# Optimization experiments

Hardware: AMD Instinct MI355X
Metric: run time of the kernel (lower is better)

The kernel has to match this reference:

```python
import jax, jax.numpy as jnp
import numpy as np

RADIUS = 1.0 / 16.0
MAX_NEIGHBORS = 64  # forward() passes max_num_neighbors=64
N_POINTS = 16384
N_CLOUDS = 8


def _radius_neighbors(pos, batch, r, k):
    """Dense radius graph: for each point, up to k in-radius same-cloud neighbors.
    Returns idx [N,k] int32 and mask [N,k] bool. loop=True -> self always valid."""
    sq = jnp.sum(pos * pos, axis=-1)                        # [N]
    d2 = sq[:, None] + sq[None, :] - 2.0 * (pos @ pos.T)    # [N,N]
    d2 = jnp.maximum(d2, 0.0)
    valid = (d2 <= r * r) & (batch[:, None] == batch[None, :])
    score = jnp.where(valid, -d2, -jnp.inf)
    vals, idx = jax.lax.top_k(score, k)                     # nearest-first, [N,k]
    mask = vals > -jnp.inf
    return idx, mask


def _point_conv(x, pos, idx, mask, W1, b1, W2, b2):
    """PointNetConv: msg = relu(Linear([x_j, pos_j - pos_i])), max-agg, Linear."""
    xj = x[idx]                                   # [N,K,c_in]  gather
    rel = pos[idx] - pos[:, None, :]              # [N,K,3]
    h = jnp.concatenate([xj, rel], axis=-1) @ W1 + b1   # [N,K,c_mid]
    h = jax.nn.relu(h)
    h = jnp.where(mask[..., None], h, -jnp.inf)
    agg = jnp.max(h, axis=1)                      # [N,c_mid]  max aggregation
    agg = jnp.where(jnp.isfinite(agg), agg, 0.0)  # safety (loop=True makes this moot)
    return agg @ W2 + b2                          # [N,c_out]


def setup_inputs() -> dict:
    key = jax.random.key(0)
    ks = jax.random.split(key, 16)
    pos = jax.random.uniform(ks[0], (N_POINTS, 3), dtype=jnp.float32)
    rgb = jax.random.uniform(ks[1], (N_POINTS, 3), dtype=jnp.float32)
    batch = jnp.sort(jax.random.randint(ks[2], (N_POINTS,), 0, N_CLOUDS)).astype(jnp.int64)

    def lin(k, fan_in, fan_out):
        kw, kb = jax.random.split(k)
        bound = 1.0 / np.sqrt(fan_in)
        W = jax.random.uniform(kw, (fan_in, fan_out), jnp.float32, -bound, bound)
        b = jax.random.uniform(kb, (fan_out,), jnp.float32, -bound, bound)
        return W, b

    W1a, b1a = lin(ks[3], 3 + 3, 8)
    W2a, b2a = lin(ks[4], 8, 8)
    W1b, b1b = lin(ks[5], 8 + 3, 16)
    W2b, b2b = lin(ks[6], 16, 16)
    W1c, b1c = lin(ks[7], 16 + 3, 32)
    W2c, b2c = lin(ks[8], 32, 32)
    return {"pos": pos, "rgb": rgb, "batch": batch,
            "W1a": W1a, "b1a": b1a, "W2a": W2a, "b2a": b2a,
            "W1b": W1b, "b1b": b1b, "W2b": W2b, "b2b": b2b,
            "W1c": W1c, "b1c": b1c, "W2c": W2c, "b2c": b2c}


def reference(pos, rgb, batch,
              W1a, b1a, W2a, b2a,
              W1b, b1b, W2b, b2b,
              W1c, b1c, W2c, b2c):
    # NOTE: rgb is accepted by the original forward() but never used.
    idx, mask = _radius_neighbors(pos, batch, RADIUS, MAX_NEIGHBORS)
    out = jax.nn.celu(_point_conv(pos, pos, idx, mask, W1a, b1a, W2a, b2a))
    out = jax.nn.celu(_point_conv(out, pos, idx, mask, W1b, b1b, W2b, b2b))
    out = jax.nn.celu(_point_conv(out, pos, idx, mask, W1c, b1c, W2c, b2c))
    return pos, out, batch
```

## Files before the change

kernel.cpp:

```cpp
#include <hip/hip_runtime.h>
#include <math.h>

#define N_POINTS 16384
#define CELLS_PER_CLOUD 4096
#define N_CELLS 32768
#define CAP 16
#define NBR_STRIDE 32

constexpr double R2D = 1.0 / 256.0;

__global__ __launch_bounds__(256) void k_prep(const float* __restrict__ pos,
                                              const int* __restrict__ batch,
                                              float* __restrict__ out,
                                              int* __restrict__ cnt,
                                              float4* __restrict__ bucket,
                                              float4* __restrict__ pos4)
{
    int i = blockIdx.x * 256 + threadIdx.x;
    out[i]                = pos[i];
    out[i + N_POINTS]     = pos[i + N_POINTS];
    out[i + 2 * N_POINTS] = pos[i + 2 * N_POINTS];
    out[3 * N_POINTS + 32 * N_POINTS + i] = (float)batch[i];

    float x = pos[3 * i], y = pos[3 * i + 1], z = pos[3 * i + 2];
    int ix = min(max((int)(x * 16.f), 0), 15);
    int iy = min(max((int)(y * 16.f), 0), 15);
    int iz = min(max((int)(z * 16.f), 0), 15);
    int cell = ((batch[i] * 16 + iz) * 16 + iy) * 16 + ix;
    pos4[i] = make_float4(x, y, z, __int_as_float(cell));
    int slot = atomicAdd(&cnt[cell], 1);
    if (slot < CAP) bucket[cell * CAP + slot] = make_float4(x, y, z, __int_as_float(i));
}

__global__ __launch_bounds__(64) void k_search_a(
    const float4* __restrict__ pos4,
    const int* __restrict__ cnt, const float4* __restrict__ bucket,
    const float* __restrict__ W1, const float* __restrict__ b1,
    const float* __restrict__ W2, const float* __restrict__ b2,
    float* __restrict__ out_a, float4* __restrict__ nbr, int* __restrict__ nbr_cnt)
{
    __shared__ float sW1[48], sB1[8], sW2[64], sB2[8];
    __shared__ float4 s_hits[NBR_STRIDE][64];
    int t = threadIdx.x;
    if (t < 48) sW1[t] = W1[t];
    if (t < 8) { sB1[t] = b1[t]; sB2[t] = b2[t]; }
    sW2[t] = W2[t];
    __syncthreads();

    int i = blockIdx.x * 64 + t;
    float4 pi4 = pos4[i];
    float xi = pi4.x, yi = pi4.y, zi = pi4.z;
    double xd = (double)xi, yd = (double)yi, zd = (double)zi;
    int cell0 = __float_as_int(pi4.w);
    int ix = cell0 & 15, iy = (cell0 >> 4) & 15, iz = (cell0 >> 8) & 15;
    int cb = cell0 & ~(CELLS_PER_CLOUD - 1);

    int n[27], cid[27];
#pragma unroll
    for (int c = 0; c < 27; c++) {
        int dz = c / 9 - 1, dy = (c / 3) % 3 - 1, dx = c % 3 - 1;
        int zz = iz + dz, yy = iy + dy, xx = ix + dx;
        bool ok = ((zz | yy | xx) >= 0) & (zz < 16) & (yy < 16) & (xx < 16);
        int zc = min(max(zz, 0), 15), yc = min(max(yy, 0), 15),
            xc = min(max(xx, 0), 15);
        cid[c] = cb + (zc << 8) + (yc << 4) + xc;
        int nc = min(cnt[cid[c]], CAP);
        n[c] = ok ? nc : 0;
    }
    int nmax = 0;
#pragma unroll
    for (int c = 0; c < 27; c++) nmax = max(nmax, n[c]);

    int k = 0;
    for (int s = 0; s < nmax; s++) {
#pragma unroll
        for (int c = 0; c < 27; c++) {
            if (s < n[c]) {
                float4 q = bucket[cid[c] * CAP + s];
                double ddx = xd - (double)q.x, ddy = yd - (double)q.y,
                       ddz = zd - (double)q.z;
                double d2 = ddx * ddx + ddy * ddy + ddz * ddz;
                if (d2 <= R2D) {
                    if (k < NBR_STRIDE) s_hits[k][t] = q;
                    k++;
                }
            }
        }
    }
    int kc = min(k, NBR_STRIDE);
    nbr_cnt[i] = kc;

    float mx[8];
#pragma unroll
    for (int m = 0; m < 8; m++) mx[m] = 0.f;
    for (int kk = 0; kk < kc; kk++) {
        float4 q = s_hits[kk][t];
        nbr[i * NBR_STRIDE + kk] = q;
        float in6[6] = { q.x, q.y, q.z, q.x - xi, q.y - yi, q.z - zi };
#pragma unroll
        for (int m = 0; m < 8; m++) {
            float h = sB1[m];
#pragma unroll
            for (int c6 = 0; c6 < 6; c6++) h = fmaf(in6[c6], sW1[c6 * 8 + m], h);
            mx[m] = fmaxf(mx[m], fmaxf(h, 0.f));
        }
    }

#pragma unroll
    for (int m = 0; m < 8; m++) {
        float o = sB2[m];
#pragma unroll
        for (int kk = 0; kk < 8; kk++) o = fmaf(mx[kk], sW2[kk * 8 + m], o);
        out_a[i * 8 + m] = o > 0.f ? o : expm1f(o);
    }
}

template<int CIN4, int CMID, int PTS>
__global__ __launch_bounds__(256) void k_conv(
    const float4* __restrict__ pos4, const float4* __restrict__ xin4,
    const float4* __restrict__ nbr, const int* __restrict__ nbr_cnt,
    const float* __restrict__ W1, const float* __restrict__ b1,
    const float* __restrict__ W2, const float* __restrict__ b2,
    float* __restrict__ xout)
{
    constexpr int CIN = CIN4 * 4;
    __shared__ float s_agg[PTS * CMID];
    int p = threadIdx.x / CMID;
    int m = threadIdx.x % CMID;
    int i = blockIdx.x * PTS + p;

    float4 pi = pos4[i];
    int cnt = nbr_cnt[i];

    float w1c[CIN + 3];
#pragma unroll
    for (int k = 0; k < CIN + 3; k++) w1c[k] = W1[k * CMID + m];
    float w2c[CMID];
#pragma unroll
    for (int k = 0; k < CMID; k++) w2c[k] = W2[k * CMID + m];
    float bb = b1[m];

    float mxv = 0.f;
    for (int t = 0; t < cnt; t++) {
        float4 q = nbr[i * NBR_STRIDE + t];
        int j = __float_as_int(q.w);
        float h = bb;
#pragma unroll
        for (int k = 0; k < CIN4; k++) {
            float4 v = xin4[j * CIN4 + k];
            h = fmaf(v.x, w1c[4 * k],     h);
            h = fmaf(v.y, w1c[4 * k + 1], h);
            h = fmaf(v.z, w1c[4 * k + 2], h);
            h = fmaf(v.w, w1c[4 * k + 3], h);
        }
        h = fmaf(q.x - pi.x, w1c[CIN],     h);
        h = fmaf(q.y - pi.y, w1c[CIN + 1], h);
        h = fmaf(q.z - pi.z, w1c[CIN + 2], h);
        mxv = fmaxf(mxv, fmaxf(h, 0.f));
    }
    s_agg[p * CMID + m] = mxv;
    __syncthreads();

    float o = b2[m];
#pragma unroll
    for (int k = 0; k < CMID; k++) o = fmaf(s_agg[p * CMID + k], w2c[k], o);
    xout[i * CMID + m] = o > 0.f ? o : expm1f(o);
}

extern "C" void kernel_launch(void* const* d_in, const int* in_sizes, int n_in,
                              void* d_out, int out_size, void* d_ws, size_t ws_size,
                              hipStream_t stream)
{
    const float* pos   = (const float*)d_in[0];
    const int*   batch = (const int*)d_in[2];
    const float* W1a = (const float*)d_in[3];
    const float* b1a = (const float*)d_in[4];
    const float* W2a = (const float*)d_in[5];
    const float* b2a = (const float*)d_in[6];
    const float* W1b = (const float*)d_in[7];
    const float* b1b = (const float*)d_in[8];
    const float* W2b = (const float*)d_in[9];
    const float* b2b = (const float*)d_in[10];
    const float* W1c = (const float*)d_in[11];
    const float* b1c = (const float*)d_in[12];
    const float* W2c = (const float*)d_in[13];
    const float* b2c = (const float*)d_in[14];

    float* out = (float*)d_out;

    char* ws = (char*)d_ws;
    size_t off = 0;
    auto alloc = [&](size_t bytes) {
        char* p = ws + off; off += (bytes + 255) & ~size_t(255); return p;
    };
    int*    cnt     = (int*)alloc(N_CELLS * 4);
    float4* bucket  = (float4*)alloc((size_t)N_CELLS * CAP * 16);
    float4* pos4    = (float4*)alloc(N_POINTS * 16);
    int*    nbr_cnt = (int*)alloc(N_POINTS * 4);
    float4* nbr     = (float4*)alloc((size_t)N_POINTS * NBR_STRIDE * 16);
    float*  out_a   = (float*)alloc(N_POINTS * 8 * 4);
    float*  out_b   = (float*)alloc(N_POINTS * 16 * 4);

    hipMemsetAsync(cnt, 0, N_CELLS * 4, stream);
    hipLaunchKernelGGL(k_prep, dim3(N_POINTS / 256), dim3(256), 0, stream,
                       pos, batch, out, cnt, bucket, pos4);
    hipLaunchKernelGGL(k_search_a, dim3(N_POINTS / 64), dim3(64), 0, stream,
                       pos4, cnt, bucket, W1a, b1a, W2a, b2a,
                       out_a, nbr, nbr_cnt);
    hipLaunchKernelGGL((k_conv<2, 16, 16>), dim3(N_POINTS / 16), dim3(256), 0, stream,
                       pos4, (const float4*)out_a, nbr, nbr_cnt,
                       W1b, b1b, W2b, b2b, out_b);
    hipLaunchKernelGGL((k_conv<4, 32, 8>), dim3(N_POINTS / 8), dim3(256), 0, stream,
                       pos4, (const float4*)out_b, nbr, nbr_cnt,
                       W1c, b1c, W2c, b2c, out + 3 * N_POINTS);
}
```

Before: 135.2 us.

## Split neighbor cell search across eight waves per point with shared atomics

The radius search kernel now uses 512 threads per block, with each of eight groups scanning a subset of the 27 neighbouring cells for the same 64 points. Hits are appended through a shared-memory atomic counter and written directly to the neighbour list. Only the first group then computes the first conv layer, and its output is stored with vectorised writes. This raises parallelism and occupancy for a launch that had few threads. The cost is shared atomics, a block barrier, and a neighbour order that is no longer deterministic when truncation happens.

```diff
diff --git a/kernel.cpp b/kernel.cpp
--- a/kernel.cpp
+++ b/kernel.cpp
@@ -32,7 +32,7 @@
     if (slot < CAP) bucket[cell * CAP + slot] = make_float4(x, y, z, __int_as_float(i));
 }
 
-__global__ __launch_bounds__(64) void k_search_a(
+__global__ __launch_bounds__(512) void k_search_a(
     const float4* __restrict__ pos4,
     const int* __restrict__ cnt, const float4* __restrict__ bucket,
     const float* __restrict__ W1, const float* __restrict__ b1,
@@ -41,13 +41,18 @@
 {
     __shared__ float sW1[48], sB1[8], sW2[64], sB2[8];
     __shared__ float4 s_hits[NBR_STRIDE][64];
+    __shared__ int s_k[64];
+
     int t = threadIdx.x;
+    int p = t & 63;
+    int g = t >> 6;
+
     if (t < 48) sW1[t] = W1[t];
     if (t < 8) { sB1[t] = b1[t]; sB2[t] = b2[t]; }
-    sW2[t] = W2[t];
+    if (t < 64) { sW2[t] = W2[t]; s_k[t] = 0; }
     __syncthreads();
 
-    int i = blockIdx.x * 64 + t;
+    int i = blockIdx.x * 64 + p;
     float4 pi4 = pos4[i];
     float xi = pi4.x, yi = pi4.y, zi = pi4.z;
     double xd = (double)xi, yd = (double)yi, zd = (double)zi;
@@ -55,63 +60,72 @@
     int ix = cell0 & 15, iy = (cell0 >> 4) & 15, iz = (cell0 >> 8) & 15;
     int cb = cell0 & ~(CELLS_PER_CLOUD - 1);
 
-    int n[27], cid[27];
-#pragma unroll
-    for (int c = 0; c < 27; c++) {
+    int n[4], cid[4];
+#pragma unroll
+    for (int cc = 0; cc < 4; cc++) {
+        int c = g + 8 * cc;
         int dz = c / 9 - 1, dy = (c / 3) % 3 - 1, dx = c % 3 - 1;
         int zz = iz + dz, yy = iy + dy, xx = ix + dx;
-        bool ok = ((zz | yy | xx) >= 0) & (zz < 16) & (yy < 16) & (xx < 16);
+        bool ok = (c < 27) & ((zz | yy | xx) >= 0) & (zz < 16) & (yy < 16) & (xx < 16);
         int zc = min(max(zz, 0), 15), yc = min(max(yy, 0), 15),
             xc = min(max(xx, 0), 15);
-        cid[c] = cb + (zc << 8) + (yc << 4) + xc;
-        int nc = min(cnt[cid[c]], CAP);
-        n[c] = ok ? nc : 0;
+        cid[cc] = cb + (zc << 8) + (yc << 4) + xc;
+        int nc = min(cnt[cid[cc]], CAP);
+        n[cc] = ok ? nc : 0;
     }
     int nmax = 0;
 #pragma unroll
-    for (int c = 0; c < 27; c++) nmax = max(nmax, n[c]);
-
-    int k = 0;
+    for (int cc = 0; cc < 4; cc++) nmax = max(nmax, n[cc]);
+
     for (int s = 0; s < nmax; s++) {
 #pragma unroll
-        for (int c = 0; c < 27; c++) {
-            if (s < n[c]) {
-                float4 q = bucket[cid[c] * CAP + s];
+        for (int cc = 0; cc < 4; cc++) {
+            if (s < n[cc]) {
+                float4 q = bucket[cid[cc] * CAP + s];
                 double ddx = xd - (double)q.x, ddy = yd - (double)q.y,
                        ddz = zd - (double)q.z;
                 double d2 = ddx * ddx + ddy * ddy + ddz * ddz;
                 if (d2 <= R2D) {
-                    if (k < NBR_STRIDE) s_hits[k][t] = q;
-                    k++;
+                    int slot = atomicAdd(&s_k[p], 1);
+                    if (slot < NBR_STRIDE) {
+                        s_hits[slot][p] = q;
+                        nbr[i * NBR_STRIDE + slot] = q;
+                    }
                 }
             }
         }
     }
-    int kc = min(k, NBR_STRIDE);
-    nbr_cnt[i] = kc;
-
-    float mx[8];
-#pragma unroll
-    for (int m = 0; m < 8; m++) mx[m] = 0.f;
-    for (int kk = 0; kk < kc; kk++) {
-        float4 q = s_hits[kk][t];
-        nbr[i * NBR_STRIDE + kk] = q;
-        float in6[6] = { q.x, q.y, q.z, q.x - xi, q.y - yi, q.z - zi };
+    __syncthreads();
+
+    if (g == 0) {
+        int kc = min(s_k[p], NBR_STRIDE);
+        nbr_cnt[i] = kc;
+
+        float mx[8];
+#pragma unroll
+        for (int m = 0; m < 8; m++) mx[m] = 0.f;
+        for (int kk = 0; kk < kc; kk++) {
+            float4 q = s_hits[kk][p];
+            float in6[6] = { q.x, q.y, q.z, q.x - xi, q.y - yi, q.z - zi };
+#pragma unroll
+            for (int m = 0; m < 8; m++) {
+                float h = sB1[m];
+#pragma unroll
+                for (int c6 = 0; c6 < 6; c6++) h = fmaf(in6[c6], sW1[c6 * 8 + m], h);
+                mx[m] = fmaxf(mx[m], fmaxf(h, 0.f));
+            }
+        }
+
+        float o[8];
 #pragma unroll
         for (int m = 0; m < 8; m++) {
-            float h = sB1[m];
-#pragma unroll
-            for (int c6 = 0; c6 < 6; c6++) h = fmaf(in6[c6], sW1[c6 * 8 + m], h);
-            mx[m] = fmaxf(mx[m], fmaxf(h, 0.f));
-        }
-    }
-
-#pragma unroll
-    for (int m = 0; m < 8; m++) {
-        float o = sB2[m];
-#pragma unroll
-        for (int kk = 0; kk < 8; kk++) o = fmaf(mx[kk], sW2[kk * 8 + m], o);
-        out_a[i * 8 + m] = o > 0.f ? o : expm1f(o);
+            float v = sB2[m];
+#pragma unroll
+            for (int kk = 0; kk < 8; kk++) v = fmaf(mx[kk], sW2[kk * 8 + m], v);
+            o[m] = v > 0.f ? v : expm1f(v);
+        }
+        *(float4*)&out_a[i * 8]     = make_float4(o[0], o[1], o[2], o[3]);
+        *(float4*)&out_a[i * 8 + 4] = make_float4(o[4], o[5], o[6], o[7]);
     }
 }
 
@@ -204,7 +218,7 @@
     hipMemsetAsync(cnt, 0, N_CELLS * 4, stream);
     hipLaunchKernelGGL(k_prep, dim3(N_POINTS / 256), dim3(256), 0, stream,
                        pos, batch, out, cnt, bucket, pos4);
-    hipLaunchKernelGGL(k_search_a, dim3(N_POINTS / 64), dim3(64), 0, stream,
+    hipLaunchKernelGGL(k_search_a, dim3(N_POINTS / 64), dim3(512), 0, stream,
                        pos4, cnt, bucket, W1a, b1a, W2a, b2a,
                        out_a, nbr, nbr_cnt);
     hipLaunchKernelGGL((k_conv<2, 16, 16>), dim3(N_POINTS / 16), dim3(256), 0, stream,
```

Measured after the change: 117.3 us. 1.15x faster.
